# Optimization experiments

Hardware: AMD Instinct MI355X
Metric: run time of the kernel (lower is better)

## Reference

```python
import jax, jax.numpy as jnp
import numpy as np

NUM_HEADS = 12
NUM_TASKS = 4


def setup_inputs() -> dict:
    key = jax.random.key(0)
    k1, k2, k3, k4 = jax.random.split(key, 4)
    B, N, C = 2, 2048, 768
    x = jax.random.normal(k1, (B, N, C), dtype=jnp.float32)
    # nn.Linear(dim, 3*dim, bias=False): store as [C, 3C] so y = x @ w_qkv
    w_qkv = jax.random.normal(k2, (C, 3 * C), dtype=jnp.float32) * (C ** -0.5)
    w_proj = jax.random.normal(k3, (C, C), dtype=jnp.float32) * (C ** -0.5)
    b_proj = jax.random.normal(k4, (C,), dtype=jnp.float32) * 0.01
    return {"x": x, "w_qkv": w_qkv, "w_proj": w_proj, "b_proj": b_proj}


def reference(x, w_qkv, w_proj, b_proj):
    B, N, C = x.shape
    H = NUM_HEADS
    d = C // H
    scale = d ** -0.5
    qkv = (x @ w_qkv).reshape(B, N, 3, H, d)
    qkv = jnp.transpose(qkv, (2, 0, 3, 1, 4))  # [3, B, H, N, d]
    q, k, v = qkv[0], qkv[1], qkv[2]
    attn = jnp.einsum("bhnd,bhmd->bhnm", q, k) * scale
    attn = jax.nn.softmax(attn, axis=-1)
    # static task mask: zero cross-task attention among first NUM_TASKS tokens
    mask = jnp.ones((N, N), dtype=attn.dtype).at[:NUM_TASKS, :NUM_TASKS].set(
        jnp.eye(NUM_TASKS, dtype=attn.dtype))
    attn = attn * mask  # broadcasts over [B, H, N, N]
    out = jnp.einsum("bhnm,bhmd->bhnd", attn, v)
    out = jnp.transpose(out, (0, 2, 1, 3)).reshape(B, N, C)
    return out @ w_proj + b_proj
```

## Files before the change

### kernel.cpp

```cpp
#include <hip/hip_runtime.h>

typedef __attribute__((ext_vector_type(4))) float f32x4;
typedef __attribute__((ext_vector_type(8))) __bf16 bf16x8;
typedef __attribute__((ext_vector_type(4))) __bf16 bf16x4;

#define QSCALE (0.125f * 1.4426950408889634f)

#define WAITV4 do { asm volatile("s_waitcnt vmcnt(4)" ::: "memory"); \
  __builtin_amdgcn_sched_barrier(0); __builtin_amdgcn_s_barrier(); \
  __builtin_amdgcn_sched_barrier(0); } while (0)
#define WAITV0 do { asm volatile("s_waitcnt vmcnt(0)" ::: "memory"); \
  __builtin_amdgcn_sched_barrier(0); __builtin_amdgcn_s_barrier(); \
  __builtin_amdgcn_sched_barrier(0); } while (0)

__device__ __forceinline__ void load_lds16(const void* g, void* l) {
  __builtin_amdgcn_global_load_lds(
      (const __attribute__((address_space(1))) unsigned int*)g,
      (__attribute__((address_space(3))) unsigned int*)l, 16, 0, 0);
}

__device__ __forceinline__ f32x4 mfma16(bf16x8 a, bf16x8 b, f32x4 c) {
  return __builtin_amdgcn_mfma_f32_16x16x32_bf16(a, b, c, 0, 0, 0);
}

__device__ __forceinline__ bf16x8 cat44(bf16x4 a, bf16x4 b) {
  return __builtin_shufflevector(a, b, 0, 1, 2, 3, 4, 5, 6, 7);
}


__global__ __launch_bounds__(256) void k_cast_x(const float* __restrict__ in,
                                                __bf16* __restrict__ out) {
  int i = blockIdx.x * 256 + threadIdx.x;
  const f32x4* in4 = (const f32x4*)in;
  f32x4 a = in4[i * 2], b = in4[i * 2 + 1];
  bf16x8 o;
  o[0] = (__bf16)a[0]; o[1] = (__bf16)a[1]; o[2] = (__bf16)a[2]; o[3] = (__bf16)a[3];
  o[4] = (__bf16)b[0]; o[5] = (__bf16)b[1]; o[6] = (__bf16)b[2]; o[7] = (__bf16)b[3];
  *(bf16x8*)(out + (size_t)i * 8) = o;
}

__global__ void k_transpose_cast(const float* __restrict__ in, __bf16* __restrict__ out,
                                 int R, int C) {
  __shared__ float t[32][33];
  int c0 = blockIdx.x * 32, r0 = blockIdx.y * 32;
  int tx = threadIdx.x, ty = threadIdx.y;
#pragma unroll
  for (int j = 0; j < 32; j += 8)
    t[ty + j][tx] = in[(size_t)(r0 + ty + j) * C + c0 + tx];
  __syncthreads();
#pragma unroll
  for (int j = 0; j < 32; j += 8)
    out[(size_t)(c0 + ty + j) * R + r0 + tx] = (__bf16)t[tx][ty + j];
}


__device__ __forceinline__ void gemm_core24(const char* aB, const char* bB,
                                            char* smem, int tid, int l,
                                            int wr, int wc, f32x4 (&acc)[4][4]) {
  auto stage = [&](int buf, int kt) {
#pragma unroll
    for (int is = 0; is < 2; ++is) {
      int o = is * 4096 + tid * 16;
      int row = o >> 6, cb = (o >> 4) & 3;
      int src = row * 1536 + (((cb ^ row) & 3) << 4) + kt * 64;
      load_lds16(aB + src, smem + buf * 8192 + o);
      load_lds16(bB + src, smem + 24576 + buf * 8192 + o);
    }
  };
  auto compute = [&](int buf) {
    const __bf16* As = (const __bf16*)(smem + buf * 8192);
    const __bf16* Bs = (const __bf16*)(smem + 24576 + buf * 8192);
    bf16x8 af[4], bfr[4];
#pragma unroll
    for (int mf = 0; mf < 4; ++mf) {
      int row = wr * 64 + mf * 16 + (l & 15);
      af[mf] = *(const bf16x8*)&As[row * 32 + ((((l >> 4) ^ row) & 3) << 3)];
    }
#pragma unroll
    for (int nf = 0; nf < 4; ++nf) {
      int row = wc * 64 + nf * 16 + (l & 15);
      bfr[nf] = *(const bf16x8*)&Bs[row * 32 + ((((l >> 4) ^ row) & 3) << 3)];
    }
    __builtin_amdgcn_s_setprio(1);
#pragma unroll
    for (int mf = 0; mf < 4; ++mf)
#pragma unroll
      for (int nf = 0; nf < 4; ++nf)
        acc[mf][nf] = mfma16(af[mf], bfr[nf], acc[mf][nf]);
    __builtin_amdgcn_s_setprio(0);
  };
  stage(0, 0); stage(1, 1);
#pragma unroll 3
  for (int t = 0; t < 21; ++t) {
    WAITV4;
    stage((t + 2) % 3, t + 2);
    compute(t % 3);
  }
  WAITV4; stage(2, 23); compute(0);
  WAITV4; compute(1);
  WAITV0; compute(2);
  __syncthreads();
}


__global__ __launch_bounds__(256, 3) void k_qkv(const __bf16* __restrict__ A,
                                                const __bf16* __restrict__ BT,
                                                __bf16* __restrict__ qb,
                                                __bf16* __restrict__ kb,
                                                __bf16* __restrict__ vT) {
  __shared__ __align__(16) char smem[49152];
  int tid = threadIdx.x, l = tid & 63, w = tid >> 6, wr = w >> 1, wc = w & 1;
  int g = l >> 4, c = l & 15;
  int m0 = blockIdx.y * 128, n0 = blockIdx.x * 128;
  f32x4 acc[4][4] = {};
  gemm_core24((const char*)(A + (size_t)m0 * 768), (const char*)(BT + (size_t)n0 * 768),
              smem, tid, l, wr, wc, acc);
  int b = m0 >> 11, m0l = m0 & 2047;
  int sel = n0 / 768;
  int rem = n0 - sel * 768;

  if (sel == 2) {
#pragma unroll
    for (int mf = 0; mf < 4; ++mf) {
      int tokb = wr * 64 + mf * 16 + 4 * g;
      int gr = tokb >> 3, low = (g & 1) << 3;
#pragma unroll
      for (int nf = 0; nf < 4; ++nf) {
        int dd = wc * 64 + nf * 16 + c;
        bf16x4 pk;
        pk[0] = (__bf16)acc[mf][nf][0]; pk[1] = (__bf16)acc[mf][nf][1];
        pk[2] = (__bf16)acc[mf][nf][2]; pk[3] = (__bf16)acc[mf][nf][3];
        *(bf16x4*)(smem + dd * 256 + (((gr ^ (dd & 15)) & 15) << 4) + low) = pk;
      }
    }
    __syncthreads();
#pragma unroll
    for (int p = 0; p < 8; ++p) {
      int idx = p * 256 + tid;
      int dd = idx >> 4, t8 = idx & 15;
      bf16x8 v = *(const bf16x8*)(smem + dd * 256 + (((t8 ^ (dd & 15)) & 15) << 4));
      int colg = rem + dd;
      int h = colg >> 6, d = colg & 63;
      *(bf16x8*)(vT + (((size_t)(b * 12 + h)) * 64 + d) * 2048 + m0l + t8 * 8) = v;
    }
  } else {
    float qs = (sel == 0) ? QSCALE : 1.0f;
#pragma unroll
    for (int mf = 0; mf < 4; ++mf)
#pragma unroll
      for (int nf = 0; nf < 4; ++nf) {
        int col = wc * 64 + nf * 16 + c;
        int grc = col >> 3, lowc = (col & 7) << 1;
#pragma unroll
        for (int r = 0; r < 4; ++r) {
          int tok = wr * 64 + mf * 16 + 4 * g + r;
          *(__bf16*)(smem + tok * 256 + (((grc ^ (tok & 15)) & 15) << 4) + lowc) =
              (__bf16)(acc[mf][nf][r] * qs);
        }
      }
    __syncthreads();
    __bf16* dst0 = (sel == 0) ? qb : kb;
#pragma unroll
    for (int p = 0; p < 8; ++p) {
      int idx = p * 256 + tid;
      int tok = idx >> 4, hh = (idx >> 3) & 1, d8 = idx & 7;
      int gr = hh * 8 + d8;
      bf16x8 v = *(const bf16x8*)(smem + tok * 256 + (((gr ^ (tok & 15)) & 15) << 4));
      int h = (rem >> 6) + hh;
      *(bf16x8*)(dst0 + (((size_t)(b * 12 + h)) * 2048 + m0l + tok) * 64 + d8 * 8) = v;
    }
  }
}


__global__ __launch_bounds__(256, 4) void k_attn(const __bf16* __restrict__ qb,
                                                 const __bf16* __restrict__ kb,
                                                 const __bf16* __restrict__ vT,
                                                 __bf16* __restrict__ Opart,
                                                 float* __restrict__ lpart) {
  __shared__ __align__(16) char smem[49152];
  int tid = threadIdx.x, l = tid & 63, w = tid >> 6;
  int g = l >> 4, c = l & 15;
  int phys = blockIdx.x;
  int lid = (phys & 7) * 96 + (phys >> 3);
  int qt = lid & 15;
  int bhsp = lid >> 4;
  int bh = bhsp % 24, sp = bhsp / 24;

  const char* qbase  = (const char*)qb + ((size_t)bh * 2048 + qt * 128) * 128;
  const char* kbase0 = (const char*)kb + (size_t)bh * 262144 + (size_t)sp * 131072;
  const char* vbase0 = (const char*)vT + (size_t)bh * 262144 + sp * 2048;

#pragma unroll
  for (int is = 0; is < 4; ++is) {
    int o = is * 4096 + tid * 16;
    int row = o >> 7, cb = (o >> 4) & 7;
    load_lds16(qbase + row * 128 + (((cb ^ row) & 7) << 4), smem + o);
  }
  __syncthreads();
  bf16x8 qf[2][2];
#pragma unroll
  for (int qi = 0; qi < 2; ++qi)
#pragma unroll
    for (int ks = 0; ks < 2; ++ks) {
      int q = w * 32 + qi * 16 + c;
      int gg = ks * 4 + g;
      qf[qi][ks] = *(const bf16x8*)(smem + q * 128 + (((gg ^ q) & 7) << 4));
    }
  __syncthreads();

  auto stageKV = [&](int buf, int t) {
    const char* kbase = kbase0 + t * 8192;
    const char* vbase = vbase0 + t * 128;
#pragma unroll
    for (int is = 0; is < 2; ++is) {
      int o = is * 4096 + tid * 16;
      int r = o >> 7, cb = (o >> 4) & 7;
      load_lds16(kbase + r * 128 + (((cb ^ r) & 7) << 4), smem + buf * 8192 + o);
      load_lds16(vbase + (size_t)r * 4096 + (((cb ^ r) & 7) << 4),
                 smem + 24576 + buf * 8192 + o);
    }
  };

  f32x4 lacc4[2] = {};
  f32x4 accO[2][4] = {};

  auto compute = [&](int t, int buf) {
    const char* KsB = smem + buf * 8192;
    const char* VsB = smem + 24576 + buf * 8192;
    const f32x4 z = {0.f, 0.f, 0.f, 0.f};
    f32x4 s[4][2];
    bf16x4 pkv[2][4];

    auto qk = [&](int kf) {
      int key = kf * 16 + c;
      const char* row = KsB + key * 128;
      bf16x8 k0 = *(const bf16x8*)(row + (((g ^ key) & 7) << 4));
      bf16x8 k1 = *(const bf16x8*)(row + ((((4 + g) ^ key) & 7) << 4));
      __builtin_amdgcn_s_setprio(1);
      s[kf][0] = mfma16(k0, qf[0][0], z);
      s[kf][1] = mfma16(k0, qf[1][0], z);
      s[kf][0] = mfma16(k1, qf[0][1], s[kf][0]);
      s[kf][1] = mfma16(k1, qf[1][1], s[kf][1]);
      __builtin_amdgcn_s_setprio(0);
    };
    auto sm = [&](int kf) {
      f32x4 p0, p1;
#pragma unroll
      for (int r = 0; r < 4; ++r) {
        p0[r] = __builtin_amdgcn_exp2f(s[kf][0][r]);
        p1[r] = __builtin_amdgcn_exp2f(s[kf][1][r]);
      }
      if (kf == 0 && sp == 0 && qt == 0 && t == 0 && w == 0 && g == 0 && c < 4) {
#pragma unroll
        for (int r = 0; r < 4; ++r)
          if (r != c) p0[r] = 0.f;
      }
      lacc4[0] += p0;
      lacc4[1] += p1;
      bf16x4 a, b;
#pragma unroll
      for (int r = 0; r < 4; ++r) { a[r] = (__bf16)p0[r]; b[r] = (__bf16)p1[r]; }
      pkv[0][kf] = a;
      pkv[1][kf] = b;
    };
    auto pv = [&](int ks2) {
      bf16x8 pa0 = cat44(pkv[0][2 * ks2], pkv[0][2 * ks2 + 1]);
      bf16x8 pa1 = cat44(pkv[1][2 * ks2], pkv[1][2 * ks2 + 1]);
      int low = (g & 1) << 3;
      int vc0 = ks2 * 4 + (g >> 1);
      __builtin_amdgcn_s_setprio(1);
#pragma unroll
      for (int df = 0; df < 4; ++df) {
        int dd = df * 16 + c;
        const char* vrow = VsB + dd * 128;
        bf16x4 v0 = *(const bf16x4*)(vrow + (((vc0 ^ dd) & 7) << 4) + low);
        bf16x4 v1 = *(const bf16x4*)(vrow + ((((vc0 + 2) ^ dd) & 7) << 4) + low);
        bf16x8 vb = cat44(v0, v1);
        accO[0][df] = mfma16(pa0, vb, accO[0][df]);
        accO[1][df] = mfma16(pa1, vb, accO[1][df]);
      }
      __builtin_amdgcn_s_setprio(0);
    };

    qk(0); qk(1);
    sm(0);
    qk(2);
    sm(1);
    pv(0);
    qk(3);
    sm(2);
    sm(3);
    pv(1);
  };

  stageKV(0, 0); stageKV(1, 1);
#pragma unroll 3
  for (int t = 0; t < 12; ++t) {
    WAITV4;
    stageKV((t + 2) % 3, t + 2);
    compute(t, t % 3);
  }
  WAITV4; stageKV(2, 14); compute(12, 0);
  WAITV4; stageKV(0, 15); compute(13, 1);
  WAITV4; compute(14, 2);
  WAITV0; compute(15, 0);
  __syncthreads();

  size_t pbase = ((size_t)sp * 24 + bh) * 2048 + qt * 128;
  float lfull[2];
#pragma unroll
  for (int qi = 0; qi < 2; ++qi) {
    float rr = lacc4[qi][0] + lacc4[qi][1] + lacc4[qi][2] + lacc4[qi][3];
    rr += __shfl_xor(rr, 16, 64);
    rr += __shfl_xor(rr, 32, 64);
    lfull[qi] = rr;
  }
  if (g == 0) {
#pragma unroll
    for (int qi = 0; qi < 2; ++qi)
      lpart[pbase + w * 32 + qi * 16 + c] = lfull[qi];
  }

  char* ep = smem + w * 4096;
#pragma unroll
  for (int mf = 0; mf < 2; ++mf) {
#pragma unroll
    for (int df = 0; df < 4; ++df) {
      int col = df * 16 + c;
      int sI = col >> 2, lowc = (col & 3) << 2;
#pragma unroll
      for (int r = 0; r < 4; ++r) {
        int rloc = 4 * g + r;
        *(float*)(ep + rloc * 256 + (((sI ^ rloc) & 15) << 4) + lowc) = accO[mf][df][r];
      }
    }
    asm volatile("s_waitcnt lgkmcnt(0)" ::: "memory");
    int rr = l >> 2, q4 = l & 3;
    f32x4 aa[4];
#pragma unroll
    for (int j = 0; j < 4; ++j) {
      int sj = q4 * 4 + j;
      aa[j] = *(const f32x4*)(ep + rr * 256 + (((sj ^ rr) & 15) << 4));
    }
    bf16x8 o0, o1;
#pragma unroll
    for (int j = 0; j < 4; ++j) { o0[j] = (__bf16)aa[0][j]; o0[4 + j] = (__bf16)aa[1][j]; }
#pragma unroll
    for (int j = 0; j < 4; ++j) { o1[j] = (__bf16)aa[2][j]; o1[4 + j] = (__bf16)aa[3][j]; }
    int q = w * 32 + mf * 16 + rr;
    char* dst = (char*)Opart + (pbase + q) * 128 + q4 * 32;
    *(bf16x8*)dst = o0;
    *(bf16x8*)(dst + 16) = o1;
  }
}


__global__ __launch_bounds__(256) void k_combine(const __bf16* __restrict__ Opart,
                                                 const float* __restrict__ lpart,
                                                 __bf16* __restrict__ ao) {
  int i = blockIdx.x * 256 + threadIdx.x;
  int d8 = i & 7, q = (i >> 3) & 2047, bh = i >> 14;
  int bg = bh / 12, h = bh - bg * 12;
  const size_t SPL = 24ull * 2048 * 64;
  size_t o0 = (((size_t)bh) * 2048 + q) * 64 + d8 * 8;
  bf16x8 a = *(const bf16x8*)(Opart + o0);
  bf16x8 b = *(const bf16x8*)(Opart + SPL + o0);
  size_t lq = (size_t)bh * 2048 + q;
  float lsum = lpart[lq] + lpart[24ull * 2048 + lq];
  float rl = __builtin_amdgcn_rcpf(lsum);
  bf16x8 o;
#pragma unroll
  for (int j = 0; j < 8; ++j)
    o[j] = (__bf16)(((float)a[j] + (float)b[j]) * rl);
  *(bf16x8*)(ao + ((size_t)bg * 2048 + q) * 768 + h * 64 + d8 * 8) = o;
}


__global__ __launch_bounds__(256, 3) void k_proj(const __bf16* __restrict__ A,
                                                 const __bf16* __restrict__ BT,
                                                 const float* __restrict__ bias,
                                                 float* __restrict__ out) {
  __shared__ __align__(16) char smem[49152];
  int tid = threadIdx.x, l = tid & 63, w = tid >> 6, wr = w >> 1, wc = w & 1;
  int m0 = blockIdx.y * 128, n0 = blockIdx.x * 128;
  f32x4 acc[4][4] = {};
  gemm_core24((const char*)(A + (size_t)m0 * 768), (const char*)(BT + (size_t)n0 * 768),
              smem, tid, l, wr, wc, acc);
#pragma unroll
  for (int nf = 0; nf < 4; ++nf) {
    int cc = n0 + wc * 64 + nf * 16 + (l & 15);
    float bi = bias[cc];
#pragma unroll
    for (int mf = 0; mf < 4; ++mf) {
      int m = m0 + wr * 64 + mf * 16 + ((l >> 4) << 2);
#pragma unroll
      for (int r = 0; r < 4; ++r)
        out[(size_t)(m + r) * 768 + cc] = acc[mf][nf][r] + bi;
    }
  }
}


extern "C" void kernel_launch(void* const* d_in, const int* in_sizes, int n_in,
                              void* d_out, int out_size, void* d_ws, size_t ws_size,
                              hipStream_t stream) {
  const float* x      = (const float*)d_in[0];
  const float* w_qkv  = (const float*)d_in[1];
  const float* w_proj = (const float*)d_in[2];
  const float* b_proj = (const float*)d_in[3];
  float* out = (float*)d_out;

  char* ws = (char*)d_ws;
  size_t off = 0;
  auto alloc = [&](size_t bytes) {
    char* p = ws + off;
    off += (bytes + 255) & ~(size_t)255;
    return p;
  };
  __bf16* xb     = (__bf16*)alloc(4096ull * 768 * 2);
  __bf16* wqkvT  = (__bf16*)alloc(2304ull * 768 * 2);
  __bf16* wprojT = (__bf16*)alloc(768ull * 768 * 2);
  __bf16* qb     = (__bf16*)alloc(24ull * 2048 * 64 * 2);
  __bf16* kb     = (__bf16*)alloc(24ull * 2048 * 64 * 2);
  __bf16* vT     = (__bf16*)alloc(24ull * 64 * 2048 * 2);
  __bf16* ao     = (__bf16*)alloc(4096ull * 768 * 2);
  __bf16* Opart  = (__bf16*)alloc(2ull * 24 * 2048 * 64 * 2);
  float*  lpart  = (float*)alloc(2ull * 24 * 2048 * 4);

  k_cast_x<<<1536, 256, 0, stream>>>(x, xb);
  k_transpose_cast<<<dim3(72, 24), dim3(32, 8), 0, stream>>>(w_qkv, wqkvT, 768, 2304);
  k_transpose_cast<<<dim3(24, 24), dim3(32, 8), 0, stream>>>(w_proj, wprojT, 768, 768);
  k_qkv<<<dim3(18, 32), 256, 0, stream>>>(xb, wqkvT, qb, kb, vT);
  k_attn<<<768, 256, 0, stream>>>(qb, kb, vT, Opart, lpart);
  k_combine<<<1536, 256, 0, stream>>>(Opart, lpart, ao);
  k_proj<<<dim3(6, 32), 256, 0, stream>>>(ao, wprojT, b_proj, out);
}
```

Baseline: 93.23 us.

## Merge weight transpose launches, precompute LDS offsets, relax barrier scheduling fences

Combines the two weight transpose-cast kernels into one launch that uses a z-dimension to pick the matrix, which removes a kernel launch. In the attention kernel, the swizzled LDS offsets for K and V fragment reads are computed once per thread outside the loop, so the inner loop only adds constant strides. It also drops the sched_barrier placed before the s_barrier in the wait macros, which gives the compiler more room to schedule. The merged launch wastes some blocks that exit early.

```diff
diff --git a/kernel.cpp b/kernel.cpp
--- a/kernel.cpp
+++ b/kernel.cpp
@@ -7,11 +7,9 @@
 #define QSCALE (0.125f * 1.4426950408889634f)
 
 #define WAITV4 do { asm volatile("s_waitcnt vmcnt(4)" ::: "memory"); \
-  __builtin_amdgcn_sched_barrier(0); __builtin_amdgcn_s_barrier(); \
-  __builtin_amdgcn_sched_barrier(0); } while (0)
+  __builtin_amdgcn_s_barrier(); __builtin_amdgcn_sched_barrier(0); } while (0)
 #define WAITV0 do { asm volatile("s_waitcnt vmcnt(0)" ::: "memory"); \
-  __builtin_amdgcn_sched_barrier(0); __builtin_amdgcn_s_barrier(); \
-  __builtin_amdgcn_sched_barrier(0); } while (0)
+  __builtin_amdgcn_s_barrier(); __builtin_amdgcn_sched_barrier(0); } while (0)
 
 __device__ __forceinline__ void load_lds16(const void* g, void* l) {
   __builtin_amdgcn_global_load_lds(
@@ -39,8 +37,13 @@
   *(bf16x8*)(out + (size_t)i * 8) = o;
 }
 
-__global__ void k_transpose_cast(const float* __restrict__ in, __bf16* __restrict__ out,
-                                 int R, int C) {
+__global__ void k_transpose_cast2(const float* __restrict__ wqkv, __bf16* __restrict__ oq,
+                                  const float* __restrict__ wproj, __bf16* __restrict__ op) {
+  int z = blockIdx.z;
+  if (z == 1 && blockIdx.x >= 24) return;
+  const float* in = z ? wproj : wqkv;
+  __bf16* out = z ? op : oq;
+  int C = z ? 768 : 2304;
   __shared__ float t[32][33];
   int c0 = blockIdx.x * 32, r0 = blockIdx.y * 32;
   int tx = threadIdx.x, ty = threadIdx.y;
@@ -50,7 +53,7 @@
   __syncthreads();
 #pragma unroll
   for (int j = 0; j < 32; j += 8)
-    out[(size_t)(c0 + ty + j) * R + r0 + tx] = (__bf16)t[tx][ty + j];
+    out[(size_t)(c0 + ty + j) * 768 + r0 + tx] = (__bf16)t[tx][ty + j];
 }
 
 
@@ -209,6 +212,14 @@
     }
   __syncthreads();
 
+  int low = (g & 1) << 3;
+  int qkoff0 = c * 128 + (((g ^ c) & 7) << 4);
+  int qkoff1 = c * 128 + ((((4 + g) ^ c) & 7) << 4);
+  int vA0 = c * 128 + ((((g >> 1) ^ c) & 7) << 4) + low;
+  int vB0 = c * 128 + ((((2 + (g >> 1)) ^ c) & 7) << 4) + low;
+  int vA1 = c * 128 + ((((4 + (g >> 1)) ^ c) & 7) << 4) + low;
+  int vB1 = c * 128 + ((((6 + (g >> 1)) ^ c) & 7) << 4) + low;
+
   auto stageKV = [&](int buf, int t) {
     const char* kbase = kbase0 + t * 8192;
     const char* vbase = vbase0 + t * 128;
@@ -226,17 +237,16 @@
   f32x4 accO[2][4] = {};
 
   auto compute = [&](int t, int buf) {
-    const char* KsB = smem + buf * 8192;
+    const char* kq0 = smem + buf * 8192 + qkoff0;
+    const char* kq1 = smem + buf * 8192 + qkoff1;
     const char* VsB = smem + 24576 + buf * 8192;
     const f32x4 z = {0.f, 0.f, 0.f, 0.f};
     f32x4 s[4][2];
     bf16x4 pkv[2][4];
 
     auto qk = [&](int kf) {
-      int key = kf * 16 + c;
-      const char* row = KsB + key * 128;
-      bf16x8 k0 = *(const bf16x8*)(row + (((g ^ key) & 7) << 4));
-      bf16x8 k1 = *(const bf16x8*)(row + ((((4 + g) ^ key) & 7) << 4));
+      bf16x8 k0 = *(const bf16x8*)(kq0 + kf * 2048);
+      bf16x8 k1 = *(const bf16x8*)(kq1 + kf * 2048);
       __builtin_amdgcn_s_setprio(1);
       s[kf][0] = mfma16(k0, qf[0][0], z);
       s[kf][1] = mfma16(k0, qf[1][0], z);
@@ -267,15 +277,13 @@
     auto pv = [&](int ks2) {
       bf16x8 pa0 = cat44(pkv[0][2 * ks2], pkv[0][2 * ks2 + 1]);
       bf16x8 pa1 = cat44(pkv[1][2 * ks2], pkv[1][2 * ks2 + 1]);
-      int low = (g & 1) << 3;
-      int vc0 = ks2 * 4 + (g >> 1);
+      const char* p0 = VsB + (ks2 ? vA1 : vA0);
+      const char* p1 = VsB + (ks2 ? vB1 : vB0);
       __builtin_amdgcn_s_setprio(1);
 #pragma unroll
       for (int df = 0; df < 4; ++df) {
-        int dd = df * 16 + c;
-        const char* vrow = VsB + dd * 128;
-        bf16x4 v0 = *(const bf16x4*)(vrow + (((vc0 ^ dd) & 7) << 4) + low);
-        bf16x4 v1 = *(const bf16x4*)(vrow + ((((vc0 + 2) ^ dd) & 7) << 4) + low);
+        bf16x4 v0 = *(const bf16x4*)(p0 + df * 2048);
+        bf16x4 v1 = *(const bf16x4*)(p1 + df * 2048);
         bf16x8 vb = cat44(v0, v1);
         accO[0][df] = mfma16(pa0, vb, accO[0][df]);
         accO[1][df] = mfma16(pa1, vb, accO[1][df]);
@@ -429,8 +437,7 @@
   float*  lpart  = (float*)alloc(2ull * 24 * 2048 * 4);
 
   k_cast_x<<<1536, 256, 0, stream>>>(x, xb);
-  k_transpose_cast<<<dim3(72, 24), dim3(32, 8), 0, stream>>>(w_qkv, wqkvT, 768, 2304);
-  k_transpose_cast<<<dim3(24, 24), dim3(32, 8), 0, stream>>>(w_proj, wprojT, 768, 768);
+  k_transpose_cast2<<<dim3(72, 24, 2), dim3(32, 8), 0, stream>>>(w_qkv, wqkvT, w_proj, wprojT);
   k_qkv<<<dim3(18, 32), 256, 0, stream>>>(xb, wqkvT, qb, kb, vT);
   k_attn<<<768, 256, 0, stream>>>(qb, kb, vT, Opart, lpart);
   k_combine<<<1536, 256, 0, stream>>>(Opart, lpart, ao);
```

New measurement: 91.41 us. No clear change (-2.0%).
